# Performance work log

Measured on AMD Instinct MI355X. Metric: run time of the kernel, lower is better.

## Reference

```python
import jax, jax.numpy as jnp
import numpy as np

N_NODES = 100000
N_EDGES = 1600000
D_IN = 128
CH = [128, 128]
N_GRAPHS = 256


def _glorot(key, shape):
    lim = float(np.sqrt(6.0 / (shape[0] + shape[1])))
    return jax.random.uniform(key, shape, jnp.float32, -lim, lim)


def setup_inputs() -> dict:
    key = jax.random.key(0)
    ks = jax.random.split(key, 12)
    x = jax.random.normal(ks[0], (N_NODES, D_IN), jnp.float32)
    edge_index = jax.random.randint(ks[1], (2, N_EDGES), 0, N_NODES, jnp.int64)
    batch = jnp.sort(jax.random.randint(ks[2], (N_NODES,), 0, N_GRAPHS, jnp.int64))
    W1 = _glorot(ks[3], (D_IN, CH[0]))
    b1 = jnp.zeros((CH[0],), jnp.float32)
    W2 = _glorot(ks[4], (CH[0], CH[1]))
    b2 = jnp.zeros((CH[1],), jnp.float32)
    Wm1 = _glorot(ks[5], (CH[1], 500)); bm1 = jnp.zeros((500,), jnp.float32)
    Wm2 = _glorot(ks[6], (500, 100));   bm2 = jnp.zeros((100,), jnp.float32)
    Wm3 = _glorot(ks[7], (100, 1));     bm3 = jnp.zeros((1,), jnp.float32)
    return {"x": x, "edge_index": edge_index, "batch": batch,
            "W1": W1, "b1": b1, "W2": W2, "b2": b2,
            "Wm1": Wm1, "bm1": bm1, "Wm2": Wm2, "bm2": bm2,
            "Wm3": Wm3, "bm3": bm3}


def gcn_conv(x, W, b, src, dst, n_nodes):
    # GCNConv with add_self_loops=True, symmetric normalization.
    h = x @ W  # [N, C]
    deg = jnp.zeros((n_nodes,), h.dtype).at[dst].add(1.0) + 1.0  # +1 self loop
    dinv = jax.lax.rsqrt(deg)  # deg >= 1
    norm = dinv[src] * dinv[dst]  # [E]
    agg = jnp.zeros_like(h).at[dst].add(h[src] * norm[:, None])
    agg = agg + h * (dinv * dinv)[:, None]  # self-loop term, norm = dinv[i]^2
    return agg + b


def global_mean_pool(x, batch, n_graphs):
    s = jax.ops.segment_sum(x, batch, num_segments=n_graphs)
    cnt = jax.ops.segment_sum(jnp.ones((x.shape[0],), x.dtype), batch, num_segments=n_graphs)
    return s / jnp.maximum(cnt, 1.0)[:, None]


def reference(x, edge_index, batch, W1, b1, W2, b2, Wm1, bm1, Wm2, bm2, Wm3, bm3):
    src, dst = edge_index[0], edge_index[1]
    h = jax.nn.relu(gcn_conv(x, W1, b1, src, dst, N_NODES))
    h = jax.nn.relu(gcn_conv(h, W2, b2, src, dst, N_NODES))
    g = global_mean_pool(h, batch, N_GRAPHS)  # [G, CH1]
    g = jax.nn.relu(g @ Wm1 + bm1)
    g = jax.nn.relu(g @ Wm2 + bm2)
    return g @ Wm3 + bm3  # [G, 1]
```

## Files before the change

### kernel.cpp

```cpp
#include <hip/hip_runtime.h>

#define CDIM 128
#define NGRAPH 256
#define BSH 7
#define BCAP 4096
#define NBLK 256
#define TILE 6272

typedef unsigned short bf16_t;
typedef __attribute__((ext_vector_type(8))) short bf16x8;
typedef __attribute__((ext_vector_type(4))) float f32x4;

__device__ __forceinline__ float bflo(unsigned u) { return __uint_as_float(u << 16); }
__device__ __forceinline__ float bfhi(unsigned u) { return __uint_as_float(u & 0xffff0000u); }
__device__ __forceinline__ unsigned short f2bf(float f) {
  unsigned u = __float_as_uint(f);
  u += 0x7fffu + ((u >> 16) & 1u);
  return (unsigned short)(u >> 16);
}

__global__ __launch_bounds__(1024) void k_phist(const int* __restrict__ dst,
    int* __restrict__ phist, const float* __restrict__ W1,
    const float* __restrict__ W2, bf16_t* __restrict__ Wtg1,
    bf16_t* __restrict__ Wtg2, float* __restrict__ gb, bf16_t* __restrict__ tz1,
    bf16_t* __restrict__ tz2, int N, int E, int NB) {
  __shared__ int hist[1024];
  int t = blockIdx.x, tid = threadIdx.x;
  int gidx = t * 1024 + tid;
  if (gidx < 16384) {
    int n = gidx >> 7, k = gidx & 127;
    Wtg1[n * 128 + k] = f2bf(W1[k * 128 + n]);
    Wtg2[n * 128 + k] = f2bf(W2[k * 128 + n]);
  }
  if (gidx < NGRAPH * CDIM) gb[gidx] = 0.f;
  if (gidx < 64) {
    ((unsigned*)(tz1 + (size_t)N * CDIM))[gidx] = 0u;
    ((unsigned*)(tz2 + (size_t)N * CDIM))[gidx] = 0u;
  }
  for (int i = tid; i < NB; i += 1024) hist[i] = 0;
  __syncthreads();
  int tile = (E + NBLK - 1) / NBLK;
  int lo = t * tile;
  int hi = lo + tile; if (hi > E) hi = E;
  for (int i = lo + tid; i < hi; i += 1024) atomicAdd(&hist[dst[i] >> BSH], 1);
  __syncthreads();
  for (int i = tid; i < NB; i += 1024) phist[i * NBLK + t] = hist[i];
}

__global__ __launch_bounds__(256) void k_bscan(int* __restrict__ phist,
    int* __restrict__ btot) {
  __shared__ int wsum[4];
  int b = blockIdx.x;
  int tid = threadIdx.x, lane = tid & 63, wave = tid >> 6;
  int orig = phist[b * NBLK + tid];
  int v = orig;
#pragma unroll
  for (int ofs = 1; ofs < 64; ofs <<= 1) {
    int u = __shfl_up(v, ofs, 64);
    if (lane >= ofs) v += u;
  }
  if (lane == 63) wsum[wave] = v;
  __syncthreads();
  int add = 0;
#pragma unroll
  for (int w = 0; w < 3; w++) if (w < wave) add += wsum[w];
  int incl = v + add;
  phist[b * NBLK + tid] = incl - orig;
  if (tid == 255) btot[b] = incl;
}

__global__ __launch_bounds__(1024) void k_pscatter(const int* __restrict__ src,
    const int* __restrict__ dst, const int* __restrict__ phist,
    const int* __restrict__ btot, unsigned* __restrict__ tmp, int E, int NB) {
  __shared__ int lh[1024];
  __shared__ int ls[1024];
  __shared__ int lc[1024];
  __shared__ int gb2[1024];
  __shared__ unsigned short sbkt[TILE];
  __shared__ unsigned sbuf[TILE];
  int t = blockIdx.x, tid = threadIdx.x;

  int v = (tid < NB) ? btot[tid] : 0;
  ls[tid] = v;
  __syncthreads();
  for (int ofs = 1; ofs < 1024; ofs <<= 1) {
    int u = (tid >= ofs) ? ls[tid - ofs] : 0;
    __syncthreads();
    ls[tid] += u;
    __syncthreads();
  }
  if (tid < NB) gb2[tid] = (ls[tid] - v) + phist[tid * NBLK + t];
  lh[tid] = 0;
  __syncthreads();

  int tile = (E + NBLK - 1) / NBLK;
  int lo = t * tile;
  int hi = lo + tile; if (hi > E) hi = E;
  int cnt = hi - lo;

  for (int i = tid; i < cnt; i += 1024) atomicAdd(&lh[dst[lo + i] >> BSH], 1);
  __syncthreads();
  int h = lh[tid];
  ls[tid] = h;
  __syncthreads();
  for (int ofs = 1; ofs < 1024; ofs <<= 1) {
    int u = (tid >= ofs) ? ls[tid - ofs] : 0;
    __syncthreads();
    ls[tid] += u;
    __syncthreads();
  }
  int excl = ls[tid] - h;
  __syncthreads();
  ls[tid] = excl;
  lc[tid] = excl;
  __syncthreads();

  for (int i = tid; i < cnt; i += 1024) {
    int d = dst[lo + i];
    int b = d >> BSH;
    unsigned pk = (unsigned)src[lo + i] | ((unsigned)(d & 127) << 20);
    int p = atomicAdd(&lc[b], 1);
    sbuf[p] = pk;
    sbkt[p] = (unsigned short)b;
  }
  __syncthreads();

  for (int j = tid; j < cnt; j += 1024) {
    int b = sbkt[j];
    tmp[gb2[b] + (j - ls[b])] = sbuf[j];
  }
}

__global__ __launch_bounds__(256) void k_csort2(const unsigned* __restrict__ tmp,
    const int* __restrict__ btot, int* __restrict__ rowptr, float* __restrict__ dinv,
    int* __restrict__ col, int N, int NB, int E) {
  __shared__ int hist[128];
  __shared__ int sc[128];
  __shared__ int lcur[128];
  __shared__ int red[256];
  __shared__ unsigned buf[BCAP];
  int b = blockIdx.x;
  int n0 = b << BSH;
  int tid = threadIdx.x;
  int part = 0;
  for (int j = tid; j < b; j += 256) part += btot[j];
  red[tid] = part;
  __syncthreads();
  for (int ofs = 128; ofs > 0; ofs >>= 1) {
    if (tid < ofs) red[tid] += red[tid + ofs];
    __syncthreads();
  }
  int base = red[0];
  int cnt = btot[b];
  if (tid < 128) hist[tid] = 0;
  __syncthreads();
  for (int i = tid; i < cnt; i += 256) atomicAdd(&hist[(tmp[base + i] >> 20) & 127], 1);
  __syncthreads();
  if (tid < 128) sc[tid] = hist[tid];
  __syncthreads();
  for (int ofs = 1; ofs < 128; ofs <<= 1) {
    int v = (tid < 128 && tid >= ofs) ? sc[tid - ofs] : 0;
    __syncthreads();
    if (tid < 128) sc[tid] += v;
    __syncthreads();
  }
  if (tid < 128) {
    int excl = sc[tid] - hist[tid];
    lcur[tid] = excl;
    int node = n0 + tid;
    if (node < N) {
      rowptr[node] = base + excl;
      dinv[node] = rsqrtf((float)hist[tid] + 1.0f);
    }
  }
  if (b == 0 && tid == 0) rowptr[N] = E;
  __syncthreads();
  if (cnt <= BCAP) {
    for (int i = tid; i < cnt; i += 256) {
      unsigned pk = tmp[base + i];
      int p = atomicAdd(&lcur[(pk >> 20) & 127], 1);
      buf[p] = pk & 0xFFFFFu;
    }
    __syncthreads();
    for (int i = tid; i < cnt; i += 256) col[base + i] = (int)buf[i];
  } else {
    for (int i = tid; i < cnt; i += 256) {
      unsigned pk = tmp[base + i];
      int p = atomicAdd(&lcur[(pk >> 20) & 127], 1);
      col[base + p] = (int)(pk & 0xFFFFFu);
    }
  }
}

#define WSTRIDE 136
template <int BF16IN>
__global__ __launch_bounds__(256) void k_gemm(const void* __restrict__ Ap,
    const bf16_t* __restrict__ Wtg, const float* __restrict__ dscale,
    bf16_t* __restrict__ Co, int M) {
  __shared__ bf16_t Wt[128 * WSTRIDE];
  int tid = threadIdx.x;
  for (int c2 = tid; c2 < 2048; c2 += 256) {
    int n = c2 >> 4;
    int k8 = (c2 & 15) << 3;
    *(uint4*)&Wt[n * WSTRIDE + k8] = *(const uint4*)&Wtg[n * 128 + k8];
  }
  __syncthreads();

  int wave = tid >> 6;
  int lane = tid & 63;
  int m = lane & 15;
  int q = lane >> 4;
  int nstrips = (M + 63) >> 6;

  for (int s = blockIdx.x; s < nstrips; s += gridDim.x) {
    int rowA = s * 64 + wave * 16 + m;
    if (rowA > M - 1) rowA = M - 1;
    bf16x8 a[4];
#pragma unroll
    for (int c = 0; c < 4; c++) {
      if (BF16IN) {
        a[c] = *(const bf16x8*)((const bf16_t*)Ap + (size_t)rowA * CDIM + c * 32 + q * 8);
      } else {
        const float* ap = (const float*)Ap + (size_t)rowA * CDIM + c * 32 + q * 8;
        float4 f0 = *(const float4*)ap;
        float4 f1 = *(const float4*)(ap + 4);
        union { bf16x8 v; unsigned short u[8]; } ua;
        ua.u[0] = f2bf(f0.x); ua.u[1] = f2bf(f0.y); ua.u[2] = f2bf(f0.z); ua.u[3] = f2bf(f0.w);
        ua.u[4] = f2bf(f1.x); ua.u[5] = f2bf(f1.y); ua.u[6] = f2bf(f1.z); ua.u[7] = f2bf(f1.w);
        a[c] = ua.v;
      }
    }
    float sc[4];
#pragma unroll
    for (int r = 0; r < 4; r++) {
      int row = s * 64 + wave * 16 + q * 4 + r;
      sc[r] = (row < M) ? dscale[row] : 0.f;
    }
#pragma unroll
    for (int t = 0; t < 8; t++) {
      f32x4 acc = {0.f, 0.f, 0.f, 0.f};
#pragma unroll
      for (int c = 0; c < 4; c++) {
        bf16x8 bv = *(const bf16x8*)&Wt[(t * 16 + m) * WSTRIDE + c * 32 + q * 8];
        acc = __builtin_amdgcn_mfma_f32_16x16x32_bf16(a[c], bv, acc, 0, 0, 0);
      }
#pragma unroll
      for (int r = 0; r < 4; r++) {
        int row = s * 64 + wave * 16 + q * 4 + r;
        if (row < M) Co[(size_t)row * CDIM + t * 16 + m] = f2bf(acc[r] * sc[r]);
      }
    }
  }
}

#define GISS(S, V, JJ) \
  { _Pragma("unroll") for (int u = 0; u < 8; u++) \
      S[u] = __builtin_amdgcn_readlane(sL, (JJ) + u); \
    _Pragma("unroll") for (int u = 0; u < 8; u++) \
      V[u] = tp[(size_t)S[u] * 64 + lane]; }
#define GCON(V) \
  { _Pragma("unroll") for (int u = 0; u < 8; u++) { \
      a0 += bflo(V[u]); a1 += bfhi(V[u]); } }
#define GBLOCK(CNT) \
  { int nb = ((CNT) + 7) >> 3; \
    GISS(sA, vA, 0); \
    int b_ = 1; \
    for (; b_ + 1 < nb; b_ += 2) { \
      GISS(sB, vB, b_ * 8);       GCON(vA); \
      GISS(sA, vA, (b_ + 1) * 8); GCON(vB); \
    } \
    if (b_ < nb) { GISS(sB, vB, b_ * 8); GCON(vA); GCON(vB); } \
    else { GCON(vA); } }

__global__ __launch_bounds__(1024) void k_aggg(const bf16_t* __restrict__ t,
    const int* __restrict__ rowptr, const int* __restrict__ col,
    const float* __restrict__ dinv, const float* __restrict__ bias,
    const bf16_t* __restrict__ Wtg, bf16_t* __restrict__ to, int N) {
  __shared__ bf16_t Wt[128 * WSTRIDE];
  __shared__ unsigned hs[64 * 68];
  int tid = threadIdx.x;
  int wave = tid >> 6, lane = tid & 63;
  for (int c2 = tid; c2 < 2048; c2 += 1024) {
    int n = c2 >> 4, k8 = (c2 & 15) << 3;
    *(uint4*)&Wt[n * WSTRIDE + k8] = *(const uint4*)&Wtg[n * 128 + k8];
  }
  const unsigned* tp = (const unsigned*)t;
  float2 bb = ((const float2*)bias)[lane];
  int sA[8]; unsigned vA[8];
  int sB[8]; unsigned vB[8];
  int nbase = blockIdx.x * 64;
#pragma unroll 1
  for (int i = 0; i < 4; i++) {
    int node = nbase + wave * 4 + i;
    unsigned hv = 0u;
    if (node < N) {
      float di = dinv[node];
      unsigned sv = tp[(size_t)node * 64 + lane];
      float a0 = bflo(sv), a1 = bfhi(sv);
      int beg = rowptr[node], end = rowptr[node + 1];
      for (int base = beg; base < end; base += 64) {
        int cnt = end - base; if (cnt > 64) cnt = 64;
        int sL = N;
        if (lane < cnt) sL = col[base + lane];
        GBLOCK(cnt);
      }
      float o0 = fmaxf(fmaf(di, a0, bb.x), 0.f);
      float o1 = fmaxf(fmaf(di, a1, bb.y), 0.f);
      hv = ((unsigned)f2bf(o1) << 16) | f2bf(o0);
    }
    hs[(wave * 4 + i) * 68 + lane] = hv;
  }
  __syncthreads();
  int rg = wave & 3, cg = wave >> 2;
  int m = lane & 15, q = lane >> 4;
  bf16x8 a[4];
#pragma unroll
  for (int c = 0; c < 4; c++)
    a[c] = *(const bf16x8*)&hs[(rg * 16 + m) * 68 + c * 16 + q * 4];
  float sc4[4]; int rows[4];
#pragma unroll
  for (int r = 0; r < 4; r++) {
    int row = nbase + rg * 16 + q * 4 + r;
    rows[r] = row;
    sc4[r] = (row < N) ? dinv[row] : 0.f;
  }
#pragma unroll
  for (int tt = 0; tt < 2; tt++) {
    int tcol = cg * 2 + tt;
    f32x4 acc = {0.f, 0.f, 0.f, 0.f};
#pragma unroll
    for (int c = 0; c < 4; c++) {
      bf16x8 bv = *(const bf16x8*)&Wt[(tcol * 16 + m) * WSTRIDE + c * 32 + q * 8];
      acc = __builtin_amdgcn_mfma_f32_16x16x32_bf16(a[c], bv, acc, 0, 0, 0);
    }
#pragma unroll
    for (int r = 0; r < 4; r++)
      if (rows[r] < N)
        to[(size_t)rows[r] * CDIM + tcol * 16 + m] = f2bf(acc[r] * sc4[r]);
  }
}

__global__ __launch_bounds__(256) void k_aggp(const bf16_t* __restrict__ t,
    const int* __restrict__ rowptr, const int* __restrict__ col,
    const float* __restrict__ dinv, const float* __restrict__ bias,
    const int* __restrict__ batch, float* __restrict__ gsum, int N) {
  int wave = threadIdx.x >> 6;
  int lane = threadIdx.x & 63;
  int n0 = (blockIdx.x * 4 + wave) * 16;
  if (n0 >= N) return;
  int nEnd = n0 + 16; if (nEnd > N) nEnd = N;
  const unsigned* tp = (const unsigned*)t;
  float2 bb = ((const float2*)bias)[lane];
  float p0 = 0.f, p1 = 0.f;
  int curb = batch[n0];
  int sA[8]; unsigned vA[8];
  int sB[8]; unsigned vB[8];

  for (int node = n0; node < nEnd; node++) {
    float di = dinv[node];
    unsigned sv = tp[(size_t)node * 64 + lane];
    float a0 = bflo(sv);
    float a1 = bfhi(sv);
    int beg = rowptr[node], end = rowptr[node + 1];
    for (int base = beg; base < end; base += 64) {
      int cnt = end - base; if (cnt > 64) cnt = 64;
      int sL = N;
      if (lane < cnt) sL = col[base + lane];
      GBLOCK(cnt);
    }
    float o0 = fmaxf(fmaf(di, a0, bb.x), 0.f);
    float o1 = fmaxf(fmaf(di, a1, bb.y), 0.f);
    int b = batch[node];
    if (b != curb) {
      atomicAdd(&gsum[curb * CDIM + 2 * lane], p0);
      atomicAdd(&gsum[curb * CDIM + 2 * lane + 1], p1);
      curb = b; p0 = p1 = 0.f;
    }
    p0 += __uint_as_float((unsigned)f2bf(o0) << 16);
    p1 += __uint_as_float((unsigned)f2bf(o1) << 16);
  }
  atomicAdd(&gsum[curb * CDIM + 2 * lane], p0);
  atomicAdd(&gsum[curb * CDIM + 2 * lane + 1], p1);
}

__global__ __launch_bounds__(512) void k_mlp(const float* __restrict__ g,
    const int* __restrict__ batch, int N,
    const float* __restrict__ Wm1, const float* __restrict__ bm1,
    const float* __restrict__ Wm2, const float* __restrict__ bm2,
    const float* __restrict__ wm3, const float* __restrict__ bm3,
    float* __restrict__ out) {
  __shared__ float gs[CDIM];
  __shared__ float m1s[500];
  __shared__ float m2s[100];
  int bi = blockIdx.x, tid = threadIdx.x;
  if (tid < CDIM) {
    int lo = 0, hi = N;
    while (lo < hi) { int mid = (lo + hi) >> 1; if (batch[mid] < bi) lo = mid + 1; else hi = mid; }
    int s = lo;
    lo = 0; hi = N;
    int key = bi + 1;
    while (lo < hi) { int mid = (lo + hi) >> 1; if (batch[mid] < key) lo = mid + 1; else hi = mid; }
    float inv = 1.f / fmaxf((float)(lo - s), 1.f);
    gs[tid] = g[bi * CDIM + tid] * inv;
  }
  __syncthreads();
  if (tid < 500) {
    float acc = bm1[tid];
#pragma unroll 4
    for (int k = 0; k < CDIM; k++) acc = fmaf(gs[k], Wm1[k * 500 + tid], acc);
    m1s[tid] = fmaxf(acc, 0.f);
  }
  __syncthreads();
  if (tid < 100) {
    float acc = bm2[tid];
    for (int k = 0; k < 500; k++) acc = fmaf(m1s[k], Wm2[k * 100 + tid], acc);
    m2s[tid] = fmaxf(acc, 0.f) * wm3[tid];
  }
  __syncthreads();
  if (tid < 64) {
    float v = m2s[tid] + ((tid + 64 < 100) ? m2s[tid + 64] : 0.f);
#pragma unroll
    for (int ofs = 32; ofs > 0; ofs >>= 1) v += __shfl_down(v, ofs, 64);
    if (tid == 0) out[bi] = v + bm3[0];
  }
}

static inline size_t align_up(size_t v) { return (v + 255) & ~(size_t)255; }

extern "C" void kernel_launch(void* const* d_in, const int* in_sizes, int n_in,
                              void* d_out, int out_size, void* d_ws, size_t ws_size,
                              hipStream_t stream) {
  const float* x   = (const float*)d_in[0];
  const int*   ei  = (const int*)d_in[1];
  const int*   bat = (const int*)d_in[2];
  const float* W1  = (const float*)d_in[3];
  const float* b1  = (const float*)d_in[4];
  const float* W2  = (const float*)d_in[5];
  const float* b2  = (const float*)d_in[6];
  const float* Wm1 = (const float*)d_in[7];
  const float* bm1 = (const float*)d_in[8];
  const float* Wm2 = (const float*)d_in[9];
  const float* bm2 = (const float*)d_in[10];
  const float* Wm3 = (const float*)d_in[11];
  const float* bm3 = (const float*)d_in[12];
  float* out = (float*)d_out;

  const int E = in_sizes[1] / 2;
  const int N = in_sizes[2];
  const int* src = ei;
  const int* dst = ei + E;
  const int NB = (N + 127) >> BSH;
  const int M  = NB * NBLK;

  char* p = (char*)d_ws;
  bf16_t* t    = (bf16_t*)p;   p += align_up((size_t)(N + 1) * CDIM * 2);
  bf16_t* t2   = (bf16_t*)p;   p += align_up((size_t)(N + 1) * CDIM * 2);
  int* rowptr  = (int*)p;      p += align_up((size_t)(N + 1) * 4);
  int* colx    = (int*)p;      p += align_up((size_t)E * 4);
  unsigned* tmp= (unsigned*)p; p += align_up((size_t)E * 4);
  float* dinv  = (float*)p;    p += align_up((size_t)N * 4);
  int* phist   = (int*)p;      p += align_up((size_t)M * 4);
  int* btot    = (int*)p;      p += align_up((size_t)NB * 4);
  bf16_t* Wtg1 = (bf16_t*)p;   p += align_up((size_t)CDIM * CDIM * 2);
  bf16_t* Wtg2 = (bf16_t*)p;   p += align_up((size_t)CDIM * CDIM * 2);
  float* gb    = (float*)p;    p += align_up((size_t)NGRAPH * CDIM * 4);
  (void)ws_size; (void)n_in; (void)out_size;

  k_phist<<<NBLK, 1024, 0, stream>>>(dst, phist, W1, W2, Wtg1, Wtg2, gb, t, t2, N, E, NB);
  k_bscan<<<NB, 256, 0, stream>>>(phist, btot);
  k_pscatter<<<NBLK, 1024, 0, stream>>>(src, dst, phist, btot, tmp, E, NB);
  k_csort2<<<NB, 256, 0, stream>>>(tmp, btot, rowptr, dinv, colx, N, NB, E);

  k_gemm<0><<<1024, 256, 0, stream>>>(x, Wtg1, dinv, t, N);
  k_aggg<<<(N + 63) / 64, 1024, 0, stream>>>(t, rowptr, colx, dinv, b1, Wtg2, t2, N);
  int pwaves = (N + 15) / 16;
  k_aggp<<<(pwaves + 3) / 4, 256, 0, stream>>>(t2, rowptr, colx, dinv, b2, bat, gb, N);
  k_mlp<<<NGRAPH, 512, 0, stream>>>(gb, bat, N, Wm1, bm1, Wm2, bm2, Wm3, bm3, out);
}
```

Measured before the change: 316.8 us.

## Fuse CSR build kernels into one cooperative kernel with grid syncs

The four separate CSR-construction kernels (partial histogram, bucket scan, partitioned scatter, per-bucket counting sort) are merged into one cooperative launch of 256 blocks that uses grid-wide syncs between phases and a union of shared-memory layouts. The aim is to remove kernel launch gaps and tail effects between small phases. Separately, k_aggg no longer stages W2 into LDS and reads MFMA B operands directly from global memory, which frees LDS for occupancy but adds global/L2 traffic inside the MFMA loop. The per-bucket phases now run with 1024 threads on 256 blocks looping over ~782 buckets, which cuts parallelism compared with the earlier per-bucket launches.

```diff
diff --git a/kernel.cpp b/kernel.cpp
--- a/kernel.cpp
+++ b/kernel.cpp
@@ -1,4 +1,5 @@
 #include <hip/hip_runtime.h>
+#include <hip/hip_cooperative_groups.h>
 
 #define CDIM 128
 #define NGRAPH 256
@@ -19,13 +20,29 @@
   return (unsigned short)(u >> 16);
 }
 
-__global__ __launch_bounds__(1024) void k_phist(const int* __restrict__ dst,
-    int* __restrict__ phist, const float* __restrict__ W1,
-    const float* __restrict__ W2, bf16_t* __restrict__ Wtg1,
-    bf16_t* __restrict__ Wtg2, float* __restrict__ gb, bf16_t* __restrict__ tz1,
-    bf16_t* __restrict__ tz2, int N, int E, int NB) {
-  __shared__ int hist[1024];
+union SortLds {
+  struct { int hist[1024]; } a;
+  struct { int wsum[16]; } b;
+  struct { int lh[1024]; int ls[1024]; int lc[1024]; int gb2[1024];
+           unsigned short sbkt[TILE]; unsigned sbuf[TILE]; } c;
+  struct { int hist[128]; int sc[128]; int lcur[128]; int red[1024];
+           unsigned buf[BCAP]; } d;
+};
+
+__global__ __launch_bounds__(1024) void k_sort(
+    const int* __restrict__ src, const int* __restrict__ dst,
+    int* __restrict__ phist, int* __restrict__ btot, unsigned* __restrict__ tmp,
+    const float* __restrict__ W1, const float* __restrict__ W2,
+    bf16_t* __restrict__ Wtg1, bf16_t* __restrict__ Wtg2,
+    float* __restrict__ gb, bf16_t* __restrict__ tz1, bf16_t* __restrict__ tz2,
+    int* __restrict__ rowptr, float* __restrict__ dinv, int* __restrict__ col,
+    int N, int E, int NB) {
+  __shared__ SortLds S;
+  cooperative_groups::grid_group gg = cooperative_groups::this_grid();
   int t = blockIdx.x, tid = threadIdx.x;
+  int lane = tid & 63, wave = tid >> 6;
+  int tile = (E + NBLK - 1) / NBLK;
+
   int gidx = t * 1024 + tid;
   if (gidx < 16384) {
     int n = gidx >> 7, k = gidx & 127;
@@ -37,157 +54,137 @@
     ((unsigned*)(tz1 + (size_t)N * CDIM))[gidx] = 0u;
     ((unsigned*)(tz2 + (size_t)N * CDIM))[gidx] = 0u;
   }
-  for (int i = tid; i < NB; i += 1024) hist[i] = 0;
-  __syncthreads();
-  int tile = (E + NBLK - 1) / NBLK;
-  int lo = t * tile;
-  int hi = lo + tile; if (hi > E) hi = E;
-  for (int i = lo + tid; i < hi; i += 1024) atomicAdd(&hist[dst[i] >> BSH], 1);
-  __syncthreads();
-  for (int i = tid; i < NB; i += 1024) phist[i * NBLK + t] = hist[i];
-}
-
-__global__ __launch_bounds__(256) void k_bscan(int* __restrict__ phist,
-    int* __restrict__ btot) {
-  __shared__ int wsum[4];
-  int b = blockIdx.x;
-  int tid = threadIdx.x, lane = tid & 63, wave = tid >> 6;
-  int orig = phist[b * NBLK + tid];
-  int v = orig;
-#pragma unroll
-  for (int ofs = 1; ofs < 64; ofs <<= 1) {
-    int u = __shfl_up(v, ofs, 64);
-    if (lane >= ofs) v += u;
-  }
-  if (lane == 63) wsum[wave] = v;
-  __syncthreads();
-  int add = 0;
-#pragma unroll
-  for (int w = 0; w < 3; w++) if (w < wave) add += wsum[w];
-  int incl = v + add;
-  phist[b * NBLK + tid] = incl - orig;
-  if (tid == 255) btot[b] = incl;
-}
-
-__global__ __launch_bounds__(1024) void k_pscatter(const int* __restrict__ src,
-    const int* __restrict__ dst, const int* __restrict__ phist,
-    const int* __restrict__ btot, unsigned* __restrict__ tmp, int E, int NB) {
-  __shared__ int lh[1024];
-  __shared__ int ls[1024];
-  __shared__ int lc[1024];
-  __shared__ int gb2[1024];
-  __shared__ unsigned short sbkt[TILE];
-  __shared__ unsigned sbuf[TILE];
-  int t = blockIdx.x, tid = threadIdx.x;
-
-  int v = (tid < NB) ? btot[tid] : 0;
-  ls[tid] = v;
-  __syncthreads();
-  for (int ofs = 1; ofs < 1024; ofs <<= 1) {
-    int u = (tid >= ofs) ? ls[tid - ofs] : 0;
-    __syncthreads();
-    ls[tid] += u;
-    __syncthreads();
-  }
-  if (tid < NB) gb2[tid] = (ls[tid] - v) + phist[tid * NBLK + t];
-  lh[tid] = 0;
-  __syncthreads();
-
-  int tile = (E + NBLK - 1) / NBLK;
-  int lo = t * tile;
-  int hi = lo + tile; if (hi > E) hi = E;
-  int cnt = hi - lo;
-
-  for (int i = tid; i < cnt; i += 1024) atomicAdd(&lh[dst[lo + i] >> BSH], 1);
-  __syncthreads();
-  int h = lh[tid];
-  ls[tid] = h;
-  __syncthreads();
-  for (int ofs = 1; ofs < 1024; ofs <<= 1) {
-    int u = (tid >= ofs) ? ls[tid - ofs] : 0;
-    __syncthreads();
-    ls[tid] += u;
-    __syncthreads();
-  }
-  int excl = ls[tid] - h;
-  __syncthreads();
-  ls[tid] = excl;
-  lc[tid] = excl;
-  __syncthreads();
-
-  for (int i = tid; i < cnt; i += 1024) {
-    int d = dst[lo + i];
-    int b = d >> BSH;
-    unsigned pk = (unsigned)src[lo + i] | ((unsigned)(d & 127) << 20);
-    int p = atomicAdd(&lc[b], 1);
-    sbuf[p] = pk;
-    sbkt[p] = (unsigned short)b;
-  }
-  __syncthreads();
-
-  for (int j = tid; j < cnt; j += 1024) {
-    int b = sbkt[j];
-    tmp[gb2[b] + (j - ls[b])] = sbuf[j];
-  }
-}
-
-__global__ __launch_bounds__(256) void k_csort2(const unsigned* __restrict__ tmp,
-    const int* __restrict__ btot, int* __restrict__ rowptr, float* __restrict__ dinv,
-    int* __restrict__ col, int N, int NB, int E) {
-  __shared__ int hist[128];
-  __shared__ int sc[128];
-  __shared__ int lcur[128];
-  __shared__ int red[256];
-  __shared__ unsigned buf[BCAP];
-  int b = blockIdx.x;
-  int n0 = b << BSH;
-  int tid = threadIdx.x;
-  int part = 0;
-  for (int j = tid; j < b; j += 256) part += btot[j];
-  red[tid] = part;
-  __syncthreads();
-  for (int ofs = 128; ofs > 0; ofs >>= 1) {
-    if (tid < ofs) red[tid] += red[tid + ofs];
-    __syncthreads();
-  }
-  int base = red[0];
-  int cnt = btot[b];
-  if (tid < 128) hist[tid] = 0;
-  __syncthreads();
-  for (int i = tid; i < cnt; i += 256) atomicAdd(&hist[(tmp[base + i] >> 20) & 127], 1);
-  __syncthreads();
-  if (tid < 128) sc[tid] = hist[tid];
-  __syncthreads();
-  for (int ofs = 1; ofs < 128; ofs <<= 1) {
-    int v = (tid < 128 && tid >= ofs) ? sc[tid - ofs] : 0;
-    __syncthreads();
-    if (tid < 128) sc[tid] += v;
-    __syncthreads();
-  }
-  if (tid < 128) {
-    int excl = sc[tid] - hist[tid];
-    lcur[tid] = excl;
-    int node = n0 + tid;
-    if (node < N) {
-      rowptr[node] = base + excl;
-      dinv[node] = rsqrtf((float)hist[tid] + 1.0f);
-    }
-  }
-  if (b == 0 && tid == 0) rowptr[N] = E;
-  __syncthreads();
-  if (cnt <= BCAP) {
-    for (int i = tid; i < cnt; i += 256) {
-      unsigned pk = tmp[base + i];
-      int p = atomicAdd(&lcur[(pk >> 20) & 127], 1);
-      buf[p] = pk & 0xFFFFFu;
-    }
-    __syncthreads();
-    for (int i = tid; i < cnt; i += 256) col[base + i] = (int)buf[i];
-  } else {
-    for (int i = tid; i < cnt; i += 256) {
-      unsigned pk = tmp[base + i];
-      int p = atomicAdd(&lcur[(pk >> 20) & 127], 1);
-      col[base + p] = (int)(pk & 0xFFFFFu);
+  for (int i = tid; i < NB; i += 1024) S.a.hist[i] = 0;
+  __syncthreads();
+  {
+    int lo = t * tile;
+    int hi = lo + tile; if (hi > E) hi = E;
+    for (int i = lo + tid; i < hi; i += 1024) atomicAdd(&S.a.hist[dst[i] >> BSH], 1);
+  }
+  __syncthreads();
+  for (int i = tid; i < NB; i += 1024) phist[i * NBLK + t] = S.a.hist[i];
+  gg.sync();
+
+  for (int bk = t; bk < NB; bk += NBLK) {
+    int orig = (tid < NBLK) ? phist[bk * NBLK + tid] : 0;
+    int v = orig;
+#pragma unroll
+    for (int ofs = 1; ofs < 64; ofs <<= 1) {
+      int u = __shfl_up(v, ofs, 64);
+      if (lane >= ofs) v += u;
+    }
+    if (lane == 63 && wave < 4) S.b.wsum[wave] = v;
+    __syncthreads();
+    int add = 0;
+#pragma unroll
+    for (int w = 0; w < 3; w++) if (w < wave) add += S.b.wsum[w];
+    int incl = v + add;
+    if (tid < NBLK) phist[bk * NBLK + tid] = incl - orig;
+    if (tid == 255) btot[bk] = incl;
+    __syncthreads();
+  }
+  gg.sync();
+
+  {
+    int v = (tid < NB) ? btot[tid] : 0;
+    S.c.ls[tid] = v;
+    __syncthreads();
+    for (int ofs = 1; ofs < 1024; ofs <<= 1) {
+      int u = (tid >= ofs) ? S.c.ls[tid - ofs] : 0;
+      __syncthreads();
+      S.c.ls[tid] += u;
+      __syncthreads();
+    }
+    if (tid < NB) S.c.gb2[tid] = (S.c.ls[tid] - v) + phist[tid * NBLK + t];
+    S.c.lh[tid] = 0;
+    __syncthreads();
+
+    int lo = t * tile;
+    int hi = lo + tile; if (hi > E) hi = E;
+    int cnt = hi - lo;
+    for (int i = tid; i < cnt; i += 1024) atomicAdd(&S.c.lh[dst[lo + i] >> BSH], 1);
+    __syncthreads();
+    int h = S.c.lh[tid];
+    S.c.ls[tid] = h;
+    __syncthreads();
+    for (int ofs = 1; ofs < 1024; ofs <<= 1) {
+      int u = (tid >= ofs) ? S.c.ls[tid - ofs] : 0;
+      __syncthreads();
+      S.c.ls[tid] += u;
+      __syncthreads();
+    }
+    int excl = S.c.ls[tid] - h;
+    __syncthreads();
+    S.c.ls[tid] = excl;
+    S.c.lc[tid] = excl;
+    __syncthreads();
+    for (int i = tid; i < cnt; i += 1024) {
+      int d = dst[lo + i];
+      int b = d >> BSH;
+      unsigned pk = (unsigned)src[lo + i] | ((unsigned)(d & 127) << 20);
+      int p = atomicAdd(&S.c.lc[b], 1);
+      S.c.sbuf[p] = pk;
+      S.c.sbkt[p] = (unsigned short)b;
+    }
+    __syncthreads();
+    for (int j = tid; j < cnt; j += 1024) {
+      int b = S.c.sbkt[j];
+      tmp[S.c.gb2[b] + (j - S.c.ls[b])] = S.c.sbuf[j];
+    }
+  }
+  gg.sync();
+
+  for (int bk = t; bk < NB; bk += NBLK) {
+    int n0 = bk << BSH;
+    int part = 0;
+    for (int j = tid; j < bk; j += 1024) part += btot[j];
+    S.d.red[tid] = part;
+    __syncthreads();
+    for (int ofs = 512; ofs > 0; ofs >>= 1) {
+      if (tid < ofs) S.d.red[tid] += S.d.red[tid + ofs];
+      __syncthreads();
+    }
+    int base = S.d.red[0];
+    int cnt = btot[bk];
+    if (tid < 128) S.d.hist[tid] = 0;
+    __syncthreads();
+    for (int i = tid; i < cnt; i += 1024) atomicAdd(&S.d.hist[(tmp[base + i] >> 20) & 127], 1);
+    __syncthreads();
+    if (tid < 128) S.d.sc[tid] = S.d.hist[tid];
+    __syncthreads();
+    for (int ofs = 1; ofs < 128; ofs <<= 1) {
+      int v = (tid < 128 && tid >= ofs) ? S.d.sc[tid - ofs] : 0;
+      __syncthreads();
+      if (tid < 128) S.d.sc[tid] += v;
+      __syncthreads();
+    }
+    if (tid < 128) {
+      int excl = S.d.sc[tid] - S.d.hist[tid];
+      S.d.lcur[tid] = excl;
+      int node = n0 + tid;
+      if (node < N) {
+        rowptr[node] = base + excl;
+        dinv[node] = rsqrtf((float)S.d.hist[tid] + 1.0f);
+      }
+    }
+    if (bk == 0 && tid == 0) rowptr[N] = E;
+    __syncthreads();
+    if (cnt <= BCAP) {
+      for (int i = tid; i < cnt; i += 1024) {
+        unsigned pk = tmp[base + i];
+        int p = atomicAdd(&S.d.lcur[(pk >> 20) & 127], 1);
+        S.d.buf[p] = pk & 0xFFFFFu;
+      }
+      __syncthreads();
+      for (int i = tid; i < cnt; i += 1024) col[base + i] = (int)S.d.buf[i];
+      __syncthreads();
+    } else {
+      for (int i = tid; i < cnt; i += 1024) {
+        unsigned pk = tmp[base + i];
+        int p = atomicAdd(&S.d.lcur[(pk >> 20) & 127], 1);
+        col[base + p] = (int)(pk & 0xFFFFFu);
+      }
+      __syncthreads();
     }
   }
 }
@@ -276,14 +273,9 @@
     const int* __restrict__ rowptr, const int* __restrict__ col,
     const float* __restrict__ dinv, const float* __restrict__ bias,
     const bf16_t* __restrict__ Wtg, bf16_t* __restrict__ to, int N) {
-  __shared__ bf16_t Wt[128 * WSTRIDE];
   __shared__ unsigned hs[64 * 68];
   int tid = threadIdx.x;
   int wave = tid >> 6, lane = tid & 63;
-  for (int c2 = tid; c2 < 2048; c2 += 1024) {
-    int n = c2 >> 4, k8 = (c2 & 15) << 3;
-    *(uint4*)&Wt[n * WSTRIDE + k8] = *(const uint4*)&Wtg[n * 128 + k8];
-  }
   const unsigned* tp = (const unsigned*)t;
   float2 bb = ((const float2*)bias)[lane];
   int sA[8]; unsigned vA[8];
@@ -330,7 +322,7 @@
     f32x4 acc = {0.f, 0.f, 0.f, 0.f};
 #pragma unroll
     for (int c = 0; c < 4; c++) {
-      bf16x8 bv = *(const bf16x8*)&Wt[(tcol * 16 + m) * WSTRIDE + c * 32 + q * 8];
+      bf16x8 bv = *(const bf16x8*)&Wtg[(tcol * 16 + m) * 128 + c * 32 + q * 8];
       acc = __builtin_amdgcn_mfma_f32_16x16x32_bf16(a[c], bv, acc, 0, 0, 0);
     }
 #pragma unroll
@@ -466,10 +458,14 @@
   float* gb    = (float*)p;    p += align_up((size_t)NGRAPH * CDIM * 4);
   (void)ws_size; (void)n_in; (void)out_size;
 
-  k_phist<<<NBLK, 1024, 0, stream>>>(dst, phist, W1, W2, Wtg1, Wtg2, gb, t, t2, N, E, NB);
-  k_bscan<<<NB, 256, 0, stream>>>(phist, btot);
-  k_pscatter<<<NBLK, 1024, 0, stream>>>(src, dst, phist, btot, tmp, E, NB);
-  k_csort2<<<NB, 256, 0, stream>>>(tmp, btot, rowptr, dinv, colx, N, NB, E);
+  int Nv = N, Ev = E, NBv = NB;
+  void* sargs[] = {
+    (void*)&src, (void*)&dst, (void*)&phist, (void*)&btot, (void*)&tmp,
+    (void*)&W1, (void*)&W2, (void*)&Wtg1, (void*)&Wtg2, (void*)&gb,
+    (void*)&t, (void*)&t2, (void*)&rowptr, (void*)&dinv, (void*)&colx,
+    (void*)&Nv, (void*)&Ev, (void*)&NBv };
+  hipLaunchCooperativeKernel((const void*)k_sort, dim3(NBLK), dim3(1024),
+                             sargs, 0, stream);
 
   k_gemm<0><<<1024, 256, 0, stream>>>(x, Wtg1, dinv, t, N);
   k_aggg<<<(N + 63) / 64, 1024, 0, stream>>>(t, rowptr, colx, dinv, b1, Wtg2, t2, N);
```

Measured after the change: 473.1 us. +49.3%, slower.
